# Kernel optimization log

Hardware: AMD Instinct MI355X
Metric: run time of the kernel (lower is better)

## Reference

```python
import jax, jax.numpy as jnp
import numpy as np

WS = 7          # window_size
HEADS = 6
HEAD_DIM = 32
DISP = WS // 2  # displacement = 3
NEG = -1e9      # stands in for -inf in shift masks (safe for grads/low precision)


def _rel_indices():
    # get_relative_distances(window_size) + window_size - 1
    pos = np.array([[i, j] for i in range(WS) for j in range(WS)])  # (49, 2)
    return pos[None, :, :] - pos[:, None, :] + WS - 1               # (49, 49, 2)


def _shift_mask(nw_h, nw_w):
    # per-window additive mask replicating upper_lower_mask / left_right_mask placement
    n = WS * WS
    ul = np.zeros((n, n), np.float32)
    ul[-DISP * WS:, :-DISP * WS] = NEG
    ul[:-DISP * WS, -DISP * WS:] = NEG
    m4 = np.zeros((WS, WS, WS, WS), np.float32)
    m4[:, -DISP:, :, :-DISP] = NEG
    m4[:, :-DISP, :, -DISP:] = NEG
    lr = m4.reshape(n, n)
    full = np.zeros((nw_h, nw_w, n, n), np.float32)
    full[-1, :] += ul              # dots[:, :, -nw_w:] += upper_lower_mask
    full[:, -1] += lr              # dots[:, :, nw_w-1::nw_w] += left_right_mask
    return full.reshape(nw_h * nw_w, n, n)


def setup_inputs() -> dict:
    key = jax.random.key(0)
    k1, k2, k3, k4 = jax.random.split(key, 4)
    dim, inner = 192, HEADS * HEAD_DIM
    return {
        "x": jax.random.normal(k1, (16, 56, 56, dim), jnp.float32),
        "w_qkv": jax.random.normal(k2, (dim, inner * 3), jnp.float32) * 0.02,
        "pos_embedding": jax.random.normal(k3, (2 * WS - 1, 2 * WS - 1), jnp.float32),
        "w_out": jax.random.normal(k4, (inner, dim), jnp.float32) * 0.02,
        "b_out": jnp.zeros((dim,), jnp.float32),
    }


def reference(x, w_qkv, pos_embedding, w_out, b_out):
    b, H, W, dim = x.shape
    nw_h, nw_w = H // WS, W // WS
    x = jnp.roll(x, (-DISP, -DISP), axis=(1, 2))          # shifted window
    qkv = x @ w_qkv                                       # [b,H,W,3*inner]
    q, k, v = jnp.split(qkv, 3, axis=-1)

    def to_windows(t):  # [b,H,W,inner] -> [b,h,nw,ws*ws,d]
        t = t.reshape(b, nw_h, WS, nw_w, WS, HEADS, HEAD_DIM)
        return t.transpose(0, 5, 1, 3, 2, 4, 6).reshape(b, HEADS, nw_h * nw_w, WS * WS, HEAD_DIM)

    q, k, v = to_windows(q), to_windows(k), to_windows(v)
    scale = HEAD_DIM ** -0.5
    dots = jnp.einsum('bhwid,bhwjd->bhwij', q, k) * scale  # [b,h,nw,49,49]

    rel = _rel_indices()
    bias = pos_embedding[rel[..., 0], rel[..., 1]]         # [49,49]
    dots = dots + bias
    dots = dots + jnp.asarray(_shift_mask(nw_h, nw_w))     # broadcast over b,h

    attn = jax.nn.softmax(dots, axis=-1)
    out = jnp.einsum('bhwij,bhwjd->bhwid', attn, v)        # [b,h,nw,49,d]
    out = out.reshape(b, HEADS, nw_h, nw_w, WS, WS, HEAD_DIM)
    out = out.transpose(0, 2, 4, 3, 5, 1, 6).reshape(b, H, W, HEADS * HEAD_DIM)
    out = out @ w_out + b_out
    return jnp.roll(out, (DISP, DISP), axis=(1, 2))
```

## Files before the change

kernel.cpp:

```cpp
#include <hip/hip_runtime.h>
#include <hip/hip_bf16.h>

typedef __bf16 bf16_t;
typedef __bf16 bf16x8 __attribute__((ext_vector_type(8)));
typedef float f32x4 __attribute__((ext_vector_type(4)));
typedef unsigned int u32;

#define NB 16
#define HW 56
#define DIM 192
#define N3 576
#define WS7 7
#define HEADS 6
#define HD 32
#define NTOK 49
#define MFMA(a, b, c) __builtin_amdgcn_mfma_f32_16x16x32_bf16(a, b, c, 0, 0, 0)

__device__ __forceinline__ void gld_lds16(const bf16_t* g, bf16_t* l) {
    __builtin_amdgcn_global_load_lds((const __attribute__((address_space(1))) u32*)g,
                                     (__attribute__((address_space(3))) u32*)l, 16, 0, 0);
}

__global__ __launch_bounds__(256) void prep_x_kernel(const float* __restrict__ x,
                                                     bf16_t* __restrict__ xb) {
    int idx = blockIdx.x * 256 + threadIdx.x;
    const int total = NB * HW * HW * (DIM / 8);
    if (idx >= total) return;
    int c8 = idx % (DIM / 8);
    int p  = idx / (DIM / 8);
    int xx = p % HW;
    int yy = (p / HW) % HW;
    int bb = p / (HW * HW);
    int ys = yy + 3; if (ys >= HW) ys -= HW;
    int xs = xx + 3; if (xs >= HW) xs -= HW;
    const float* src = x + ((size_t)(bb * HW + ys) * HW + xs) * DIM + c8 * 8;
    float4 a0 = *reinterpret_cast<const float4*>(src);
    float4 a1 = *reinterpret_cast<const float4*>(src + 4);
    bf16x8 o;
    o[0] = (bf16_t)a0.x; o[1] = (bf16_t)a0.y; o[2] = (bf16_t)a0.z; o[3] = (bf16_t)a0.w;
    o[4] = (bf16_t)a1.x; o[5] = (bf16_t)a1.y; o[6] = (bf16_t)a1.z; o[7] = (bf16_t)a1.w;
    *reinterpret_cast<bf16x8*>(xb + (size_t)idx * 8) = o;
}

__global__ __launch_bounds__(256) void prep_w_kernel(const float* __restrict__ wqkv,
                                                     const float* __restrict__ wout,
                                                     bf16_t* __restrict__ wqkvt,
                                                     bf16_t* __restrict__ woutt) {
    int idx = blockIdx.x * 256 + threadIdx.x;
    if (idx < N3 * DIM) {
        int k = idx % DIM, n = idx / DIM;
        wqkvt[idx] = (bf16_t)wqkv[(size_t)k * N3 + n];
    } else {
        int j = idx - N3 * DIM;
        if (j < DIM * DIM) {
            int k = j % DIM, n = j / DIM;
            woutt[j] = (bf16_t)wout[(size_t)k * DIM + n];
        }
    }
}

__global__ __launch_bounds__(256) void prep_tbl_kernel(const float* __restrict__ pe,
                                                       float* __restrict__ tbl) {
    int idx = blockIdx.x * 256 + threadIdx.x;
    if (idx >= 4 * 64 * 64) return;
    int v = idx >> 12, rem = idx & 4095, ti = rem >> 6, tj = rem & 63;
    float val = -1e9f;
    if (ti < NTOK && tj < NTOK) {
        int yi = ti / 7, xi = ti % 7, yj = tj / 7, xj = tj % 7;
        val = pe[(yj - yi + 6) * 13 + (xj - xi + 6)];
        bool mr = (v & 2) && ((yi >= 4) != (yj >= 4));
        bool mc = (v & 1) && ((xi >= 4) != (xj >= 4));
        if (mr || mc) val = -1e9f;
    }
    tbl[idx] = val;
}

__global__ __launch_bounds__(256) void qkv_gemm3(const bf16_t* __restrict__ xb,
                                                 const bf16_t* __restrict__ wt,
                                                 bf16_t* __restrict__ qkv) {
    __shared__ alignas(16) bf16_t bsh[64 * DIM];
    const int mblk = blockIdx.x, nblk = blockIdx.y;
    const int wave = threadIdx.x >> 6, lane = threadIdx.x & 63;
    const int lo = lane & 15, hi = lane >> 4;

    const bf16_t* bt = wt + (size_t)nblk * 64 * DIM;
#pragma unroll
    for (int i = 0; i < 6; i++) {
        int s = wave * 384 + i * 64 + lane;
        int g = s ^ ((s / 24) & 7);
        gld_lds16(bt + g * 8, bsh + (wave * 384 + i * 64) * 8);
    }

    bf16x8 a[4][6];
    const bf16_t* ab = xb + ((size_t)mblk * 256 + wave * 64 + lo) * DIM + hi * 8;
#pragma unroll
    for (int mt = 0; mt < 4; mt++)
#pragma unroll
        for (int ks = 0; ks < 6; ks++)
            a[mt][ks] = *reinterpret_cast<const bf16x8*>(ab + mt * 16 * DIM + ks * 32);

    f32x4 acc[4][4];
#pragma unroll
    for (int mt = 0; mt < 4; mt++)
#pragma unroll
        for (int ct = 0; ct < 4; ct++) acc[mt][ct] = (f32x4){0.f, 0.f, 0.f, 0.f};

    __syncthreads();

#pragma unroll
    for (int ks = 0; ks < 6; ks++)
#pragma unroll
        for (int ct = 0; ct < 4; ct++) {
            int r = ct * 16 + lo;
            int off = (ks * 64 + hi * 16) ^ ((r & 7) << 4);
            bf16x8 b = *reinterpret_cast<const bf16x8*>((const char*)bsh + r * 384 + off);
#pragma unroll
            for (int mt = 0; mt < 4; mt++)
                acc[mt][ct] = MFMA(a[mt][ks], b, acc[mt][ct]);
        }

    const float qs = (nblk < 3) ? 0.17677669529663687f : 1.0f;
    const size_t rb = (size_t)mblk * 256 + wave * 64;
#pragma unroll
    for (int mt = 0; mt < 4; mt++)
#pragma unroll
        for (int ct = 0; ct < 4; ct++)
#pragma unroll
            for (int r = 0; r < 4; r++)
                qkv[(rb + mt * 16 + hi * 4 + r) * N3 + nblk * 64 + ct * 16 + lo] =
                    (bf16_t)(acc[mt][ct][r] * qs);
}

__global__ __launch_bounds__(64) void attn_kernel3(const bf16_t* __restrict__ qkv,
                                                   const float* __restrict__ tbl,
                                                   bf16_t* __restrict__ att) {
    const int win = blockIdx.x, h = blockIdx.y, bb = blockIdx.z;
    const int wh = win >> 3, ww = win & 7;
    const int lane = threadIdx.x;
    const int lo = lane & 15, hi = lane >> 4;

    __shared__ bf16_t P[64][72];
    __shared__ alignas(16) bf16_t VT[32][72];

    const float* tv = tbl + (((wh == 7) ? 2 : 0 | 0) + ((wh == 7) ? 0 : 0), 0);
    const int variant = ((wh == 7) ? 2 : 0) | ((ww == 7) ? 1 : 0);
    const float* tbase = tbl + ((size_t)variant << 12);
    (void)tv;

    auto tokoff = [&](int t) -> size_t {
        int ti = t / 7, tj = t % 7;
        return ((size_t)(bb * HW + wh * WS7 + ti) * HW + ww * WS7 + tj) * N3 + h * HD;
    };

    {
        const int t = lane;
        bf16x8 v[4];
        if (t < NTOK) {
            const bf16_t* vp = qkv + tokoff(t) + 2 * DIM;
#pragma unroll
            for (int c = 0; c < 4; c++) v[c] = *reinterpret_cast<const bf16x8*>(vp + c * 8);
        } else {
#pragma unroll
            for (int c = 0; c < 4; c++)
#pragma unroll
                for (int j = 0; j < 8; j++) v[c][j] = (bf16_t)0.f;
        }
#pragma unroll
        for (int c = 0; c < 4; c++)
#pragma unroll
            for (int j = 0; j < 8; j++) VT[c * 8 + j][t] = v[c][j];
    }
    __syncthreads();

    bf16x8 qf[4], kf[4];
#pragma unroll
    for (int t4 = 0; t4 < 4; t4++) {
        int t = t4 * 16 + lo;
        if (t < NTOK) {
            size_t off = tokoff(t) + hi * 8;
            qf[t4] = *reinterpret_cast<const bf16x8*>(qkv + off);
            kf[t4] = *reinterpret_cast<const bf16x8*>(qkv + off + DIM);
        } else {
#pragma unroll
            for (int j = 0; j < 8; j++) { qf[t4][j] = (bf16_t)0.f; kf[t4][j] = (bf16_t)0.f; }
        }
    }

    const f32x4 zero4 = {0.f, 0.f, 0.f, 0.f};
    f32x4 s[4][4];
#pragma unroll
    for (int mt = 0; mt < 4; mt++)
#pragma unroll
        for (int ct = 0; ct < 4; ct++)
            s[mt][ct] = MFMA(qf[mt], kf[ct], zero4);

    float rinv[4][4];
#pragma unroll
    for (int mt = 0; mt < 4; mt++) {
#pragma unroll
        for (int r = 0; r < 4; r++) {
            int ti = mt * 16 + hi * 4 + r;
            const float* trow = tbase + ti * 64 + lo;
            float vals[4];
            float mx = -3e38f;
#pragma unroll
            for (int ct = 0; ct < 4; ct++) {
                float v = s[mt][ct][r] + trow[ct * 16];
                vals[ct] = v;
                mx = fmaxf(mx, v);
            }
#pragma unroll
            for (int off = 1; off < 16; off <<= 1) mx = fmaxf(mx, __shfl_xor(mx, off));
            float sum = 0.f;
#pragma unroll
            for (int ct = 0; ct < 4; ct++) {
                float p = __expf(vals[ct] - mx);
                sum += p;
                P[ti][ct * 16 + lo] = (bf16_t)p;
            }
#pragma unroll
            for (int off = 1; off < 16; off <<= 1) sum += __shfl_xor(sum, off);
            rinv[mt][r] = 1.f / sum;
        }
    }
    __syncthreads();

    f32x4 o[4][2];
#pragma unroll
    for (int mt = 0; mt < 4; mt++)
#pragma unroll
        for (int c2 = 0; c2 < 2; c2++) o[mt][c2] = zero4;

#pragma unroll
    for (int ks = 0; ks < 2; ks++) {
        bf16x8 vb[2];
#pragma unroll
        for (int c2 = 0; c2 < 2; c2++)
            vb[c2] = *reinterpret_cast<const bf16x8*>(&VT[c2 * 16 + lo][ks * 32 + hi * 8]);
#pragma unroll
        for (int mt = 0; mt < 4; mt++) {
            bf16x8 pa = *reinterpret_cast<const bf16x8*>(&P[mt * 16 + lo][ks * 32 + hi * 8]);
#pragma unroll
            for (int c2 = 0; c2 < 2; c2++)
                o[mt][c2] = MFMA(pa, vb[c2], o[mt][c2]);
        }
    }

#pragma unroll
    for (int mt = 0; mt < 4; mt++) {
#pragma unroll
        for (int r = 0; r < 4; r++) {
            int ti = mt * 16 + hi * 4 + r;
            if (ti < NTOK) {
                int y = wh * WS7 + ti / 7, x = ww * WS7 + ti % 7;
                size_t aoff = ((size_t)(bb * HW + y) * HW + x) * DIM + h * HD;
#pragma unroll
                for (int c2 = 0; c2 < 2; c2++)
                    att[aoff + c2 * 16 + lo] = (bf16_t)(o[mt][c2][r] * rinv[mt][r]);
            }
        }
    }
}

__global__ __launch_bounds__(256) void out_gemm2(const bf16_t* __restrict__ att,
                                                 const bf16_t* __restrict__ wt,
                                                 const float* __restrict__ bias,
                                                 float* __restrict__ out) {
    __shared__ alignas(16) bf16_t bsh[64 * DIM];
    const int mblk = blockIdx.x, nblk = blockIdx.y;
    const int wave = threadIdx.x >> 6, lane = threadIdx.x & 63;
    const int lo = lane & 15, hi = lane >> 4;

    const bf16_t* bt = wt + (size_t)nblk * 64 * DIM;
#pragma unroll
    for (int i = 0; i < 6; i++) {
        int s = wave * 384 + i * 64 + lane;
        int g = s ^ ((s / 24) & 7);
        gld_lds16(bt + g * 8, bsh + (wave * 384 + i * 64) * 8);
    }

    bf16x8 a[2][6];
    const bf16_t* ab = att + ((size_t)mblk * 128 + wave * 32 + lo) * DIM + hi * 8;
#pragma unroll
    for (int mt = 0; mt < 2; mt++)
#pragma unroll
        for (int ks = 0; ks < 6; ks++)
            a[mt][ks] = *reinterpret_cast<const bf16x8*>(ab + mt * 16 * DIM + ks * 32);

    f32x4 acc[2][4];
#pragma unroll
    for (int mt = 0; mt < 2; mt++)
#pragma unroll
        for (int ct = 0; ct < 4; ct++) acc[mt][ct] = (f32x4){0.f, 0.f, 0.f, 0.f};

    __syncthreads();

#pragma unroll
    for (int ks = 0; ks < 6; ks++)
#pragma unroll
        for (int ct = 0; ct < 4; ct++) {
            int r = ct * 16 + lo;
            int off = (ks * 64 + hi * 16) ^ ((r & 7) << 4);
            bf16x8 b = *reinterpret_cast<const bf16x8*>((const char*)bsh + r * 384 + off);
            acc[0][ct] = MFMA(a[0][ks], b, acc[0][ct]);
            acc[1][ct] = MFMA(a[1][ks], b, acc[1][ct]);
        }

    const int rb = mblk * 128 + wave * 32;
#pragma unroll
    for (int mt = 0; mt < 2; mt++)
#pragma unroll
        for (int r = 0; r < 4; r++) {
            int m = rb + mt * 16 + hi * 4 + r;
            int bb = m / (HW * HW);
            int rem = m - bb * HW * HW;
            int ya = rem / HW, xa = rem - ya * HW;
            int yo = ya + 3; if (yo >= HW) yo -= HW;
            int xo = xa + 3; if (xo >= HW) xo -= HW;
            size_t ob = ((size_t)(bb * HW + yo) * HW + xo) * DIM + nblk * 64;
#pragma unroll
            for (int ct = 0; ct < 4; ct++)
                out[ob + ct * 16 + lo] = acc[mt][ct][r] + bias[nblk * 64 + ct * 16 + lo];
        }
}

extern "C" void kernel_launch(void* const* d_in, const int* in_sizes, int n_in,
                              void* d_out, int out_size, void* d_ws, size_t ws_size,
                              hipStream_t stream) {
    const float* x    = (const float*)d_in[0];
    const float* wqkv = (const float*)d_in[1];
    const float* pe   = (const float*)d_in[2];
    const float* wout = (const float*)d_in[3];
    const float* bout = (const float*)d_in[4];
    float* out = (float*)d_out;

    char* ws = (char*)d_ws;
    const size_t XB_BYTES  = (size_t)NB * HW * HW * DIM * 2;
    const size_t QKV_BYTES = (size_t)NB * HW * HW * N3 * 2;
    const size_t ATT_BYTES = XB_BYTES;
    const size_t WQ_BYTES  = (size_t)N3 * DIM * 2;
    const size_t WO_BYTES  = (size_t)DIM * DIM * 2;
    bf16_t* xb    = (bf16_t*)ws;
    bf16_t* qkv   = (bf16_t*)(ws + XB_BYTES);
    bf16_t* att   = (bf16_t*)(ws + XB_BYTES + QKV_BYTES);
    bf16_t* wqkvt = (bf16_t*)(ws + XB_BYTES + QKV_BYTES + ATT_BYTES);
    bf16_t* woutt = (bf16_t*)(ws + XB_BYTES + QKV_BYTES + ATT_BYTES + WQ_BYTES);
    float*  tbl   = (float*)(ws + XB_BYTES + QKV_BYTES + ATT_BYTES + WQ_BYTES + WO_BYTES);

    prep_x_kernel<<<(NB * HW * HW * (DIM / 8) + 255) / 256, 256, 0, stream>>>(x, xb);
    prep_w_kernel<<<(N3 * DIM + DIM * DIM + 255) / 256, 256, 0, stream>>>(wqkv, wout, wqkvt, woutt);
    prep_tbl_kernel<<<64, 256, 0, stream>>>(pe, tbl);
    qkv_gemm3<<<dim3(196, 9), 256, 0, stream>>>(xb, wqkvt, qkv);
    attn_kernel3<<<dim3(64, HEADS, NB), 64, 0, stream>>>(qkv, tbl, att);
    out_gemm2<<<dim3(392, 3), 256, 0, stream>>>(att, woutt, bout, out);
}
```

Baseline: 180.3 us.

## Fuse roll+bf16 cast into QKV GEMM and split attention across four waves

```diff
diff --git a/kernel.cpp b/kernel.cpp
--- a/kernel.cpp
+++ b/kernel.cpp
@@ -19,27 +19,6 @@
 __device__ __forceinline__ void gld_lds16(const bf16_t* g, bf16_t* l) {
     __builtin_amdgcn_global_load_lds((const __attribute__((address_space(1))) u32*)g,
                                      (__attribute__((address_space(3))) u32*)l, 16, 0, 0);
-}
-
-__global__ __launch_bounds__(256) void prep_x_kernel(const float* __restrict__ x,
-                                                     bf16_t* __restrict__ xb) {
-    int idx = blockIdx.x * 256 + threadIdx.x;
-    const int total = NB * HW * HW * (DIM / 8);
-    if (idx >= total) return;
-    int c8 = idx % (DIM / 8);
-    int p  = idx / (DIM / 8);
-    int xx = p % HW;
-    int yy = (p / HW) % HW;
-    int bb = p / (HW * HW);
-    int ys = yy + 3; if (ys >= HW) ys -= HW;
-    int xs = xx + 3; if (xs >= HW) xs -= HW;
-    const float* src = x + ((size_t)(bb * HW + ys) * HW + xs) * DIM + c8 * 8;
-    float4 a0 = *reinterpret_cast<const float4*>(src);
-    float4 a1 = *reinterpret_cast<const float4*>(src + 4);
-    bf16x8 o;
-    o[0] = (bf16_t)a0.x; o[1] = (bf16_t)a0.y; o[2] = (bf16_t)a0.z; o[3] = (bf16_t)a0.w;
-    o[4] = (bf16_t)a1.x; o[5] = (bf16_t)a1.y; o[6] = (bf16_t)a1.z; o[7] = (bf16_t)a1.w;
-    *reinterpret_cast<bf16x8*>(xb + (size_t)idx * 8) = o;
 }
 
 __global__ __launch_bounds__(256) void prep_w_kernel(const float* __restrict__ wqkv,
@@ -75,7 +54,7 @@
     tbl[idx] = val;
 }
 
-__global__ __launch_bounds__(256) void qkv_gemm3(const bf16_t* __restrict__ xb,
+__global__ __launch_bounds__(256) void qkv_gemm4(const float* __restrict__ x,
                                                  const bf16_t* __restrict__ wt,
                                                  bf16_t* __restrict__ qkv) {
     __shared__ alignas(16) bf16_t bsh[64 * DIM];
@@ -92,12 +71,25 @@
     }
 
     bf16x8 a[4][6];
-    const bf16_t* ab = xb + ((size_t)mblk * 256 + wave * 64 + lo) * DIM + hi * 8;
-#pragma unroll
-    for (int mt = 0; mt < 4; mt++)
-#pragma unroll
-        for (int ks = 0; ks < 6; ks++)
-            a[mt][ks] = *reinterpret_cast<const bf16x8*>(ab + mt * 16 * DIM + ks * 32);
+#pragma unroll
+    for (int mt = 0; mt < 4; mt++) {
+        int m = mblk * 256 + wave * 64 + mt * 16 + lo;
+        int bb = m / (HW * HW);
+        int rem = m - bb * HW * HW;
+        int yy = rem / HW, xx = rem - (rem / HW) * HW;
+        int ys = yy + 3; if (ys >= HW) ys -= HW;
+        int xs = xx + 3; if (xs >= HW) xs -= HW;
+        const float* src = x + ((size_t)(bb * HW + ys) * HW + xs) * DIM + hi * 8;
+#pragma unroll
+        for (int ks = 0; ks < 6; ks++) {
+            float4 f0 = *reinterpret_cast<const float4*>(src + ks * 32);
+            float4 f1 = *reinterpret_cast<const float4*>(src + ks * 32 + 4);
+            bf16x8 o;
+            o[0] = (bf16_t)f0.x; o[1] = (bf16_t)f0.y; o[2] = (bf16_t)f0.z; o[3] = (bf16_t)f0.w;
+            o[4] = (bf16_t)f1.x; o[5] = (bf16_t)f1.y; o[6] = (bf16_t)f1.z; o[7] = (bf16_t)f1.w;
+            a[mt][ks] = o;
+        }
+    }
 
     f32x4 acc[4][4];
 #pragma unroll
@@ -131,21 +123,20 @@
                     (bf16_t)(acc[mt][ct][r] * qs);
 }
 
-__global__ __launch_bounds__(64) void attn_kernel3(const bf16_t* __restrict__ qkv,
-                                                   const float* __restrict__ tbl,
-                                                   bf16_t* __restrict__ att) {
+__global__ __launch_bounds__(256) void attn_kernel4(const bf16_t* __restrict__ qkv,
+                                                    const float* __restrict__ tbl,
+                                                    bf16_t* __restrict__ att) {
     const int win = blockIdx.x, h = blockIdx.y, bb = blockIdx.z;
     const int wh = win >> 3, ww = win & 7;
-    const int lane = threadIdx.x;
+    const int mt = threadIdx.x >> 6;
+    const int lane = threadIdx.x & 63;
     const int lo = lane & 15, hi = lane >> 4;
 
     __shared__ bf16_t P[64][72];
     __shared__ alignas(16) bf16_t VT[32][72];
 
-    const float* tv = tbl + (((wh == 7) ? 2 : 0 | 0) + ((wh == 7) ? 0 : 0), 0);
     const int variant = ((wh == 7) ? 2 : 0) | ((ww == 7) ? 1 : 0);
     const float* tbase = tbl + ((size_t)variant << 12);
-    (void)tv;
 
     auto tokoff = [&](int t) -> size_t {
         int ti = t / 7, tj = t % 7;
@@ -153,111 +144,93 @@
     };
 
     {
-        const int t = lane;
-        bf16x8 v[4];
+        const int t = mt * 16 + lo;
+        bf16x8 v;
         if (t < NTOK) {
-            const bf16_t* vp = qkv + tokoff(t) + 2 * DIM;
-#pragma unroll
-            for (int c = 0; c < 4; c++) v[c] = *reinterpret_cast<const bf16x8*>(vp + c * 8);
+            v = *reinterpret_cast<const bf16x8*>(qkv + tokoff(t) + 2 * DIM + hi * 8);
         } else {
 #pragma unroll
-            for (int c = 0; c < 4; c++)
-#pragma unroll
-                for (int j = 0; j < 8; j++) v[c][j] = (bf16_t)0.f;
-        }
-#pragma unroll
-        for (int c = 0; c < 4; c++)
-#pragma unroll
-            for (int j = 0; j < 8; j++) VT[c * 8 + j][t] = v[c][j];
-    }
+            for (int j = 0; j < 8; j++) v[j] = (bf16_t)0.f;
+        }
+#pragma unroll
+        for (int j = 0; j < 8; j++) VT[hi * 8 + j][t] = v[j];
+    }
+
+    bf16x8 qf, kf[4];
+    {
+        int t = mt * 16 + lo;
+        if (t < NTOK) {
+            qf = *reinterpret_cast<const bf16x8*>(qkv + tokoff(t) + hi * 8);
+        } else {
+#pragma unroll
+            for (int j = 0; j < 8; j++) qf[j] = (bf16_t)0.f;
+        }
+    }
+#pragma unroll
+    for (int ct = 0; ct < 4; ct++) {
+        int t = ct * 16 + lo;
+        if (t < NTOK) {
+            kf[ct] = *reinterpret_cast<const bf16x8*>(qkv + tokoff(t) + DIM + hi * 8);
+        } else {
+#pragma unroll
+            for (int j = 0; j < 8; j++) kf[ct][j] = (bf16_t)0.f;
+        }
+    }
+
+    const f32x4 zero4 = {0.f, 0.f, 0.f, 0.f};
+    f32x4 s[4];
+#pragma unroll
+    for (int ct = 0; ct < 4; ct++) s[ct] = MFMA(qf, kf[ct], zero4);
+
+    float rinv[4];
+#pragma unroll
+    for (int r = 0; r < 4; r++) {
+        int ti = mt * 16 + hi * 4 + r;
+        const float* trow = tbase + ti * 64 + lo;
+        float vals[4];
+        float mx = -3e38f;
+#pragma unroll
+        for (int ct = 0; ct < 4; ct++) {
+            float v = s[ct][r] + trow[ct * 16];
+            vals[ct] = v;
+            mx = fmaxf(mx, v);
+        }
+#pragma unroll
+        for (int off = 1; off < 16; off <<= 1) mx = fmaxf(mx, __shfl_xor(mx, off));
+        float sum = 0.f;
+#pragma unroll
+        for (int ct = 0; ct < 4; ct++) {
+            float p = __expf(vals[ct] - mx);
+            sum += p;
+            P[ti][ct * 16 + lo] = (bf16_t)p;
+        }
+#pragma unroll
+        for (int off = 1; off < 16; off <<= 1) sum += __shfl_xor(sum, off);
+        rinv[r] = 1.f / sum;
+    }
+
     __syncthreads();
 
-    bf16x8 qf[4], kf[4];
-#pragma unroll
-    for (int t4 = 0; t4 < 4; t4++) {
-        int t = t4 * 16 + lo;
-        if (t < NTOK) {
-            size_t off = tokoff(t) + hi * 8;
-            qf[t4] = *reinterpret_cast<const bf16x8*>(qkv + off);
-            kf[t4] = *reinterpret_cast<const bf16x8*>(qkv + off + DIM);
-        } else {
-#pragma unroll
-            for (int j = 0; j < 8; j++) { qf[t4][j] = (bf16_t)0.f; kf[t4][j] = (bf16_t)0.f; }
-        }
-    }
-
-    const f32x4 zero4 = {0.f, 0.f, 0.f, 0.f};
-    f32x4 s[4][4];
-#pragma unroll
-    for (int mt = 0; mt < 4; mt++)
-#pragma unroll
-        for (int ct = 0; ct < 4; ct++)
-            s[mt][ct] = MFMA(qf[mt], kf[ct], zero4);
-
-    float rinv[4][4];
-#pragma unroll
-    for (int mt = 0; mt < 4; mt++) {
-#pragma unroll
-        for (int r = 0; r < 4; r++) {
-            int ti = mt * 16 + hi * 4 + r;
-            const float* trow = tbase + ti * 64 + lo;
-            float vals[4];
-            float mx = -3e38f;
-#pragma unroll
-            for (int ct = 0; ct < 4; ct++) {
-                float v = s[mt][ct][r] + trow[ct * 16];
-                vals[ct] = v;
-                mx = fmaxf(mx, v);
-            }
-#pragma unroll
-            for (int off = 1; off < 16; off <<= 1) mx = fmaxf(mx, __shfl_xor(mx, off));
-            float sum = 0.f;
-#pragma unroll
-            for (int ct = 0; ct < 4; ct++) {
-                float p = __expf(vals[ct] - mx);
-                sum += p;
-                P[ti][ct * 16 + lo] = (bf16_t)p;
-            }
-#pragma unroll
-            for (int off = 1; off < 16; off <<= 1) sum += __shfl_xor(sum, off);
-            rinv[mt][r] = 1.f / sum;
-        }
-    }
-    __syncthreads();
-
-    f32x4 o[4][2];
-#pragma unroll
-    for (int mt = 0; mt < 4; mt++)
-#pragma unroll
-        for (int c2 = 0; c2 < 2; c2++) o[mt][c2] = zero4;
-
+    f32x4 o[2] = {zero4, zero4};
 #pragma unroll
     for (int ks = 0; ks < 2; ks++) {
-        bf16x8 vb[2];
-#pragma unroll
-        for (int c2 = 0; c2 < 2; c2++)
-            vb[c2] = *reinterpret_cast<const bf16x8*>(&VT[c2 * 16 + lo][ks * 32 + hi * 8]);
-#pragma unroll
-        for (int mt = 0; mt < 4; mt++) {
-            bf16x8 pa = *reinterpret_cast<const bf16x8*>(&P[mt * 16 + lo][ks * 32 + hi * 8]);
+        bf16x8 pa = *reinterpret_cast<const bf16x8*>(&P[mt * 16 + lo][ks * 32 + hi * 8]);
+#pragma unroll
+        for (int c2 = 0; c2 < 2; c2++) {
+            bf16x8 vb = *reinterpret_cast<const bf16x8*>(&VT[c2 * 16 + lo][ks * 32 + hi * 8]);
+            o[c2] = MFMA(pa, vb, o[c2]);
+        }
+    }
+
+#pragma unroll
+    for (int r = 0; r < 4; r++) {
+        int ti = mt * 16 + hi * 4 + r;
+        if (ti < NTOK) {
+            int y = wh * WS7 + ti / 7, xcol = ww * WS7 + ti % 7;
+            size_t aoff = ((size_t)(bb * HW + y) * HW + xcol) * DIM + h * HD;
 #pragma unroll
             for (int c2 = 0; c2 < 2; c2++)
-                o[mt][c2] = MFMA(pa, vb[c2], o[mt][c2]);
-        }
-    }
-
-#pragma unroll
-    for (int mt = 0; mt < 4; mt++) {
-#pragma unroll
-        for (int r = 0; r < 4; r++) {
-            int ti = mt * 16 + hi * 4 + r;
-            if (ti < NTOK) {
-                int y = wh * WS7 + ti / 7, x = ww * WS7 + ti % 7;
-                size_t aoff = ((size_t)(bb * HW + y) * HW + x) * DIM + h * HD;
-#pragma unroll
-                for (int c2 = 0; c2 < 2; c2++)
-                    att[aoff + c2 * 16 + lo] = (bf16_t)(o[mt][c2][r] * rinv[mt][r]);
-            }
+                att[aoff + c2 * 16 + lo] = (bf16_t)(o[c2][r] * rinv[r]);
         }
     }
 }
@@ -335,22 +308,19 @@
     float* out = (float*)d_out;
 
     char* ws = (char*)d_ws;
-    const size_t XB_BYTES  = (size_t)NB * HW * HW * DIM * 2;
     const size_t QKV_BYTES = (size_t)NB * HW * HW * N3 * 2;
-    const size_t ATT_BYTES = XB_BYTES;
+    const size_t ATT_BYTES = (size_t)NB * HW * HW * DIM * 2;
     const size_t WQ_BYTES  = (size_t)N3 * DIM * 2;
     const size_t WO_BYTES  = (size_t)DIM * DIM * 2;
-    bf16_t* xb    = (bf16_t*)ws;
-    bf16_t* qkv   = (bf16_t*)(ws + XB_BYTES);
-    bf16_t* att   = (bf16_t*)(ws + XB_BYTES + QKV_BYTES);
-    bf16_t* wqkvt = (bf16_t*)(ws + XB_BYTES + QKV_BYTES + ATT_BYTES);
-    bf16_t* woutt = (bf16_t*)(ws + XB_BYTES + QKV_BYTES + ATT_BYTES + WQ_BYTES);
-    float*  tbl   = (float*)(ws + XB_BYTES + QKV_BYTES + ATT_BYTES + WQ_BYTES + WO_BYTES);
-
-    prep_x_kernel<<<(NB * HW * HW * (DIM / 8) + 255) / 256, 256, 0, stream>>>(x, xb);
+    bf16_t* qkv   = (bf16_t*)ws;
+    bf16_t* att   = (bf16_t*)(ws + QKV_BYTES);
+    bf16_t* wqkvt = (bf16_t*)(ws + QKV_BYTES + ATT_BYTES);
+    bf16_t* woutt = (bf16_t*)(ws + QKV_BYTES + ATT_BYTES + WQ_BYTES);
+    float*  tbl   = (float*)(ws + QKV_BYTES + ATT_BYTES + WQ_BYTES + WO_BYTES);
+
     prep_w_kernel<<<(N3 * DIM + DIM * DIM + 255) / 256, 256, 0, stream>>>(wqkv, wout, wqkvt, woutt);
     prep_tbl_kernel<<<64, 256, 0, stream>>>(pe, tbl);
-    qkv_gemm3<<<dim3(196, 9), 256, 0, stream>>>(xb, wqkvt, qkv);
-    attn_kernel3<<<dim3(64, HEADS, NB), 64, 0, stream>>>(qkv, tbl, att);
+    qkv_gemm4<<<dim3(196, 9), 256, 0, stream>>>(x, wqkvt, qkv);
+    attn_kernel4<<<dim3(64, HEADS, NB), 256, 0, stream>>>(qkv, tbl, att);
     out_gemm2<<<dim3(392, 3), 256, 0, stream>>>(att, woutt, bout, out);
 }
```

Measured after the change: 198.7 us. 1.1x slower.
